# Kernel tuning notes

Measured on AMD Instinct MI355X. Metric: run time of the kernel, lower is better.

## Reference

```python
import jax, jax.numpy as jnp
import numpy as np
from jax import lax

B, C_IN, T_IN = 1024, 22, 2047
C_TEMP, KT, PAD = 20, 12, 6
N_PATCH = 8
ATT_OUT = 18
N_OUT = 4
BN_EPS = 1e-5
REEIG_EPS = 1e-4


def _sym(X):
    return 0.5 * (X + jnp.swapaxes(X, -1, -2))


def _eig_fn(X, fn):
    w, v = jnp.linalg.eigh(_sym(X))
    return jnp.einsum('...ij,...j,...kj->...ik', v, fn(w), v)


def _logm(X):
    return _eig_fn(X, lambda w: jnp.log(jnp.maximum(w, 1e-10)))


def _expm(X):
    return _eig_fn(X, jnp.exp)


def _reeig(X):
    return _eig_fn(X, lambda w: jnp.maximum(w, REEIG_EPS))


def _batchnorm(x, gamma, beta):
    # x: (B, C, T); training-mode stats over (B, T)
    mu = x.mean(axis=(0, 2), keepdims=True)
    var = x.var(axis=(0, 2), keepdims=True)
    return (x - mu) * jax.lax.rsqrt(var + BN_EPS) * gamma[None, :, None] + beta[None, :, None]


def setup_inputs() -> dict:
    key = jax.random.key(0)
    ks = jax.random.split(key, 8)
    tangent_dim = ATT_OUT * (ATT_OUT + 1) // 2
    return {
        'x': jax.random.normal(ks[0], (B, C_IN, T_IN), dtype=jnp.float32),
        'w_spat': jax.random.normal(ks[1], (C_IN, C_IN), dtype=jnp.float32) * 0.3,
        'b_spat': jnp.zeros((C_IN,), jnp.float32),
        'g1': jnp.ones((C_IN,), jnp.float32),
        'be1': jnp.zeros((C_IN,), jnp.float32),
        'w_temp': jax.random.normal(ks[2], (C_TEMP, C_IN, KT), dtype=jnp.float32) * 0.1,
        'b_temp': jnp.zeros((C_TEMP,), jnp.float32),
        'g2': jnp.ones((C_TEMP,), jnp.float32),
        'be2': jnp.zeros((C_TEMP,), jnp.float32),
        'wq': jax.random.normal(ks[3], (ATT_OUT, C_TEMP), dtype=jnp.float32) / np.sqrt(C_TEMP),
        'wk': jax.random.normal(ks[4], (ATT_OUT, C_TEMP), dtype=jnp.float32) / np.sqrt(C_TEMP),
        'wv': jax.random.normal(ks[5], (ATT_OUT, C_TEMP), dtype=jnp.float32) / np.sqrt(C_TEMP),
        'w_lin': jax.random.normal(ks[6], (N_OUT, N_PATCH * tangent_dim), dtype=jnp.float32) * 0.05,
        'b_lin': jnp.zeros((N_OUT,), jnp.float32),
    }


def _matt_forward(x, w_spat, b_spat, g1, be1, w_temp, b_temp, g2, be2, wq, wk, wv, w_lin, b_lin):
    b = x.shape[0]
    # spatial filter: Conv2d(1, n_chans, (n_chans,1)) == full channel mix
    h = jnp.einsum('oc,bct->bot', w_spat, x) + b_spat[None, :, None]
    h = _batchnorm(h, g1, be1)
    # temporal conv: Conv2d(n_chans, 20, (1,12), pad (0,6)) == 1D conv over time
    h = lax.conv_general_dilated(h, w_temp, window_strides=(1,), padding=[(PAD, PAD)],
                                 dimension_numbers=('NCH', 'OIH', 'NCH'))
    h = h + b_temp[None, :, None]
    h = _batchnorm(h, g2, be2)
    # patch embedding: split time into N_PATCH segments -> (B, P, C, Tp)
    cf, tt = h.shape[1], h.shape[2]
    tp = tt // N_PATCH
    h = h[:, :, :N_PATCH * tp].reshape(b, cf, N_PATCH, tp).transpose(0, 2, 1, 3)
    # sample covariance per patch + trace normalization
    hc = h - h.mean(axis=-1, keepdims=True)
    cov = jnp.einsum('bpct,bpdt->bpcd', hc, hc) / (tp - 1)
    cov = cov / jnp.trace(cov, axis1=-2, axis2=-1)[..., None, None]
    # manifold attention: BiMap Q/K/V = W X W^T
    Q = jnp.einsum('oi,bpij,qj->bpoq', wq, cov, wq)
    K = jnp.einsum('oi,bpij,qj->bpoq', wk, cov, wk)
    V = jnp.einsum('oi,bpij,qj->bpoq', wv, cov, wv)
    lq, lk, lv = _logm(Q), _logm(K), _logm(V)
    n = lq.shape[-1]
    fq = lq.reshape(b, N_PATCH, n * n)
    fk = lk.reshape(b, N_PATCH, n * n)
    sq = jnp.sum(fq * fq, -1)
    sk = jnp.sum(fk * fk, -1)
    cross = jnp.einsum('bid,bjd->bij', fq, fk)
    d2 = jnp.maximum(sq[:, :, None] + sk[:, None, :] - 2.0 * cross, 0.0)
    energy = jnp.sqrt(d2 + 1e-12)  # log-Euclidean distance ||logQ_i - logK_j||_F
    weights = 1.0 / (1.0 + jnp.log1p(energy))
    prob = jax.nn.softmax(weights, axis=-2)          # normalize over queries i
    probT = jnp.swapaxes(prob, -1, -2)               # (b, j, i)
    # log-Euclidean weighted Frechet mean: expm(sum_i w_ji logm(V_i))
    out = _expm(jnp.einsum('bji,bixy->bjxy', probT, lv))
    # R2E: ReEig + LogEig + triu vectorization (off-diag * sqrt(2))
    lt = _logm(_reeig(out))
    iu0, iu1 = np.triu_indices(n)
    scale = jnp.asarray(np.where(iu0 == iu1, 1.0, np.sqrt(2.0)), dtype=lt.dtype)
    vec = lt[..., iu0, iu1] * scale                  # (B, P, n(n+1)/2)
    feat = vec.reshape(b, -1)
    return feat @ w_lin.T + b_lin


def reference(x, w_spat, b_spat, g1, be1, w_temp, b_temp, g2, be2, wq, wk, wv, w_lin, b_lin):
    return _matt_forward(x, w_spat, b_spat, g1, be1, w_temp, b_temp, g2, be2, wq, wk, wv, w_lin, b_lin)
```

## Files before the change

### kernel.cpp

```cpp
#include <hip/hip_runtime.h>
#include <math.h>

constexpr int NSWEEP = 5;

constexpr size_t OFF_SUMX   = 0;
constexpr size_t OFF_G      = 22;
constexpr size_t OFF_SUM2   = 288;
constexpr size_t OFF_SUMSQ2 = 308;
constexpr size_t OFF_S2     = 328;
constexpr size_t OFF_A      = 352;
constexpr size_t OFF_D      = 840;
constexpr size_t OFF_WR     = 864;
constexpr size_t OFF_COV    = 6144;
constexpr size_t OFF_LQKV   = 3282944;
constexpr size_t OFF_FEAT   = 11245568;

struct Tri { int a[253]; int b[253]; };
constexpr Tri mk_tri(int n) {
    Tri t{}; int c = 0;
    for (int i = 0; i < n; ++i) for (int j = i; j < n; ++j) { t.a[c] = i; t.b[c] = j; ++c; }
    return t;
}
constexpr Tri T22 = mk_tri(22);
constexpr Tri T20 = mk_tri(20);
constexpr Tri T18 = mk_tri(18);

struct Sched { int p[17][9]; int q[17][9]; };
constexpr Sched mk_sched() {
    Sched s{};
    for (int r = 0; r < 17; ++r)
        for (int k = 0; k < 9; ++k) {
            int x, y;
            if (k == 0) { x = 17; y = r; }
            else { x = (r + k) % 17; y = (r - k + 17) % 17; }
            s.p[r][k] = x < y ? x : y;
            s.q[r][k] = x < y ? y : x;
        }
    return s;
}
constexpr Sched SCH = mk_sched();

__device__ __forceinline__ float jacobi18(float* __restrict__ a, float* __restrict__ v,
                                          int jj, int base) {
    int pt[17];
#pragma unroll
    for (int r = 0; r < 17; ++r) {
        int k1 = jj - r; if (k1 < 0) k1 += 17;
        int partner;
        if (jj == 17)      { partner = r; }
        else if (k1 == 0)  { partner = 17; }
        else if (k1 <= 8)  { partner = r - k1; if (partner < 0) partner += 17; }
        else               { partner = r + 17 - k1; if (partner >= 17) partner -= 17; }
        pt[r] = partner;
    }
    int kt[17];
#pragma unroll
    for (int r = 0; r < 17; ++r) {
        int k1 = jj - r; if (k1 < 0) k1 += 17;
        kt[r] = (jj == 17) ? 0 : (k1 == 0 ? 0 : (k1 <= 8 ? k1 : 17 - k1));
    }
    float mydiag = a[0];
#pragma unroll
    for (int i = 1; i < 18; ++i) if (jj == i) mydiag = a[i];

    for (int sw = 0; sw < NSWEEP; ++sw) {
#pragma unroll
        for (int r = 0; r < 17; ++r) {
            const int partner = pt[r];
            const int paddr = base + partner;
            const bool isp = jj < partner;
            float pd = __shfl(mydiag, paddr, 64);
            float apq = a[0];
#pragma unroll
            for (int i = 1; i < 18; ++i) if (partner == i) apq = a[i];
            float app = isp ? mydiag : pd;
            float aqq = isp ? pd : mydiag;
            float apqc = (fabsf(apq) < 1e-36f) ? 1e-36f : apq;
            float tau = (aqq - app) * 0.5f * __builtin_amdgcn_rcpf(apqc);
            float t0 = __builtin_amdgcn_rcpf(fabsf(tau) + __builtin_amdgcn_sqrtf(1.f + tau * tau));
            t0 = (tau < 0.f) ? -t0 : t0;
            float tb[9];
#pragma unroll
            for (int k = 0; k < 9; ++k)
                tb[k] = __shfl(t0, base + SCH.p[r][k], 64);
            float cc[9], ss[9];
#pragma unroll
            for (int k = 0; k < 9; ++k) {
                cc[k] = __builtin_amdgcn_rsqf(1.f + tb[k] * tb[k]);
                ss[k] = tb[k] * cc[k];
            }
            const int kk = kt[r];
            float mt = tb[0], mc = cc[0], ms = ss[0];
#pragma unroll
            for (int t2 = 1; t2 < 9; ++t2)
                if (kk == t2) { mt = tb[t2]; mc = cc[t2]; ms = ss[t2]; }
            mydiag = fmaf(isp ? -mt : mt, apq, mydiag);
#pragma unroll
            for (int k = 0; k < 9; ++k) {
                const int p = SCH.p[r][k], q = SCH.q[r][k];
                float tp = a[p], tq = a[q];
                a[p] = cc[k] * tp - ss[k] * tq;
                a[q] = ss[k] * tp + cc[k] * tq;
            }
            float ssig = isp ? -ms : ms;
#pragma unroll
            for (int i = 0; i < 18; ++i) {
                float oa = __shfl(a[i], paddr, 64);
                a[i] = mc * a[i] + ssig * oa;
            }
#pragma unroll
            for (int i = 0; i < 18; ++i) {
                float ov = __shfl(v[i], paddr, 64);
                v[i] = mc * v[i] + ssig * ov;
            }
        }
    }
    float lam = a[0];
#pragma unroll
    for (int i = 1; i < 18; ++i) if (jj == i) lam = a[i];
    return lam;
}

__global__ void k0_zero(float* ws) {
    int tid = threadIdx.x;
    for (int i = tid; i < 352; i += 256) ws[i] = 0.f;
}

__global__ __launch_bounds__(256) void k1_stats(const float* __restrict__ x,
                                                float* __restrict__ sumx,
                                                float* __restrict__ G) {
    int b = blockIdx.x, tid = threadIdx.x;
    __shared__ float xt[22 * 257];
    float accp = 0.f, accs = 0.f;
    int c1 = 0, c2 = 0;
    if (tid < 253) { c1 = T22.a[tid]; c2 = T22.b[tid]; }
    const float* xb = x + (size_t)b * 22 * 2047;
    for (int t0 = 0; t0 < 2047; t0 += 256) {
        __syncthreads();
        for (int idx = tid; idx < 22 * 256; idx += 256) {
            int c = idx >> 8, tl = idx & 255;
            int t = t0 + tl;
            xt[c * 257 + tl] = (t < 2047) ? xb[c * 2047 + t] : 0.f;
        }
        __syncthreads();
        if (tid < 253) {
            float s = 0.f;
            for (int t = 0; t < 256; ++t) s += xt[c1 * 257 + t] * xt[c2 * 257 + t];
            accp += s;
        }
        if (tid < 22) {
            float s = 0.f;
            for (int t = 0; t < 256; ++t) s += xt[tid * 257 + t];
            accs += s;
        }
    }
    if (tid < 253) atomicAdd(&G[tid], accp);
    if (tid < 22) atomicAdd(&sumx[tid], accs);
}

__global__ __launch_bounds__(256) void k2_prep(const float* __restrict__ w_spat,
                                               const float* __restrict__ b_spat,
                                               const float* __restrict__ g1,
                                               const float* __restrict__ be1,
                                               const float* __restrict__ w_temp,
                                               const float* __restrict__ sumx,
                                               const float* __restrict__ G,
                                               float* __restrict__ A,
                                               float* __restrict__ dv,
                                               float* __restrict__ w_r) {
    int tid = threadIdx.x;
    __shared__ float cov[22 * 22], mux[22], mu1s[22], s1s[22];
    const float invN = 1.f / (1024.f * 2047.f);
    if (tid < 22) mux[tid] = sumx[tid] * invN;
    __syncthreads();
    if (tid < 253) {
        int c1 = T22.a[tid], c2 = T22.b[tid];
        float cv = G[tid] * invN - mux[c1] * mux[c2];
        cov[c1 * 22 + c2] = cv; cov[c2 * 22 + c1] = cv;
    }
    __syncthreads();
    if (tid < 22) {
        int c = tid;
        float m = b_spat[c], varv = 0.f;
        for (int e = 0; e < 22; ++e) m += w_spat[c * 22 + e] * mux[e];
        for (int i = 0; i < 22; ++i) {
            float wi = w_spat[c * 22 + i];
            for (int j = 0; j < 22; ++j) varv += wi * w_spat[c * 22 + j] * cov[i * 22 + j];
        }
        mu1s[c] = m;
        s1s[c] = g1[c] * rsqrtf(varv + 1e-5f);
    }
    __syncthreads();
    for (int idx = tid; idx < 484; idx += 256) {
        int c = idx / 22;
        A[idx] = s1s[c] * w_spat[idx];
    }
    if (tid < 22) dv[tid] = s1s[tid] * (b_spat[tid] - mu1s[tid]) + be1[tid];
    for (int idx = tid; idx < 5280; idx += 256) {
        int f = idx / 264, r = idx % 264;
        w_r[r * 20 + f] = w_temp[idx];
    }
}

__global__ __launch_bounds__(256) void k3_conv(const float* __restrict__ x,
                                               const float* __restrict__ wsA,
                                               const float* __restrict__ wsd,
                                               const float* __restrict__ w_r,
                                               float* __restrict__ cov_raw,
                                               float* __restrict__ sum2,
                                               float* __restrict__ sumsq2) {
    int bp = blockIdx.x;
    int b = bp >> 3, p = bp & 7;
    int tid = threadIdx.x;
    __shared__ float xs[22 * 267];
    __shared__ float h2[20 * 257];
    __shared__ float pm[20];

    const float* xb = x + (size_t)b * 22 * 2047;
    const int t0 = p * 256 - 6;
    for (int idx = tid; idx < 22 * 267; idx += 256) {
        int c = idx / 267, tl = idx % 267;
        int t = t0 + tl;
        xs[idx] = (t >= 0 && t < 2047) ? xb[c * 2047 + t] : 0.f;
    }
    __syncthreads();
    for (int tl = tid; tl < 267; tl += 256) {
        float xv[22];
#pragma unroll
        for (int c = 0; c < 22; ++c) xv[c] = xs[c * 267 + tl];
        int t = t0 + tl;
        bool valid = (t >= 0 && t < 2047);
#pragma unroll
        for (int c = 0; c < 22; ++c) {
            float acc = wsd[c];
#pragma unroll
            for (int e = 0; e < 22; ++e) acc += wsA[c * 22 + e] * xv[e];
            xs[c * 267 + tl] = valid ? acc : 0.f;
        }
    }
    __syncthreads();
    {
        int tl = tid;
        float acc[20];
#pragma unroll
        for (int f = 0; f < 20; ++f) acc[f] = 0.f;
        for (int c = 0; c < 22; ++c) {
#pragma unroll
            for (int k = 0; k < 12; ++k) {
                float hv = xs[c * 267 + tl + k];
                const float* wp = w_r + (c * 12 + k) * 20;
#pragma unroll
                for (int f = 0; f < 20; ++f) acc[f] += wp[f] * hv;
            }
        }
#pragma unroll
        for (int f = 0; f < 20; ++f) h2[f * 257 + tl] = acc[f];
    }
    __syncthreads();
    if (tid < 20) {
        int f = tid;
        float s = 0.f, ss = 0.f;
        for (int t = 0; t < 256; ++t) { float v = h2[f * 257 + t]; s += v; ss += v * v; }
        pm[f] = s * (1.f / 256.f);
        atomicAdd(&sum2[f], s);
        atomicAdd(&sumsq2[f], ss);
    }
    __syncthreads();
    for (int pr = tid; pr < 210; pr += 256) {
        int f = T20.a[pr], g = T20.b[pr];
        float s = 0.f;
        for (int t = 0; t < 256; ++t) s += h2[f * 257 + t] * h2[g * 257 + t];
        float cv = s - 256.f * pm[f] * pm[g];
        cov_raw[(size_t)bp * 400 + f * 20 + g] = cv;
        if (f != g) cov_raw[(size_t)bp * 400 + g * 20 + f] = cv;
    }
}

__global__ void k4_s2(const float* __restrict__ g2, const float* __restrict__ sum2,
                      const float* __restrict__ sumsq2, float* __restrict__ s2) {
    int tid = threadIdx.x;
    if (tid < 20) {
        const float invN = 1.f / (1024.f * 2048.f);
        float mu = sum2[tid] * invN;
        float var = sumsq2[tid] * invN - mu * mu;
        s2[tid] = g2[tid] * rsqrtf(var + 1e-5f);
    }
}

__global__ __launch_bounds__(256) void k5_qkv(const float* __restrict__ wq,
                                              const float* __restrict__ wk,
                                              const float* __restrict__ wv,
                                              const float* __restrict__ s2g,
                                              const float* __restrict__ cov_raw,
                                              float* __restrict__ lqkv) {
    int tid = threadIdx.x;
    int wave = tid >> 6;
    int lane = tid & 63;
    int bp = blockIdx.x * 4 + wave;
    __shared__ float Wl[1080];
    __shared__ float s2l[20];
    __shared__ float covn[4][400];
    __shared__ float Vs[4][972];
    __shared__ float lws[4][54];

    if (tid < 20) s2l[tid] = s2g[tid];
    for (int idx = lane; idx < 400; idx += 64)
        covn[wave][idx] = cov_raw[(size_t)bp * 400 + idx];
    __syncthreads();
    for (int idx = tid; idx < 1080; idx += 256) {
        int m = idx / 360, rem = idx % 360;
        const float* W = (m == 0) ? wq : (m == 1) ? wk : wv;
        Wl[idx] = W[rem] * s2l[rem % 20];
    }
    __syncthreads();

    float tr = 0.f;
#pragma unroll
    for (int f = 0; f < 20; ++f) tr += covn[wave][f * 21] * s2l[f] * s2l[f];
    float trinv = 1.f / tr;

    int grp = lane / 18;
    int jj = lane - grp * 18;
    int m = grp < 3 ? grp : 2;
    int base = grp * 18;
    float Wrow[20];
#pragma unroll
    for (int d = 0; d < 20; ++d) Wrow[d] = Wl[m * 360 + jj * 20 + d];
    float u[20];
#pragma unroll
    for (int e = 0; e < 20; ++e) {
        float acc = 0.f;
#pragma unroll
        for (int d = 0; d < 20; ++d) acc += covn[wave][e * 20 + d] * Wrow[d];
        u[e] = acc;
    }
    float a[18], v[18];
#pragma unroll
    for (int i = 0; i < 18; ++i) {
        float acc = 0.f;
#pragma unroll
        for (int e = 0; e < 20; ++e) acc += Wl[m * 360 + i * 20 + e] * u[e];
        a[i] = acc * trinv;
        v[i] = (i == jj) ? 1.f : 0.f;
    }
    float lam = jacobi18(a, v, jj, base);
    float lw = __logf(fmaxf(lam, 1e-10f));
    if (grp < 3) {
#pragma unroll
        for (int i = 0; i < 18; ++i) Vs[wave][(m * 18 + i) * 18 + jj] = v[i];
        lws[wave][m * 18 + jj] = lw;
    }
    __builtin_amdgcn_wave_barrier();
    for (int idx = lane; idx < 972; idx += 64) {
        int m2 = idx / 324, rem = idx % 324, i = rem / 18, jo = rem % 18;
        float acc = 0.f;
#pragma unroll
        for (int kk = 0; kk < 18; ++kk)
            acc += Vs[wave][(m2 * 18 + i) * 18 + kk] * lws[wave][m2 * 18 + kk] * Vs[wave][(m2 * 18 + jo) * 18 + kk];
        lqkv[(size_t)(bp * 3 + m2) * 324 + rem] = acc;
    }
}

__global__ __launch_bounds__(256) void k6_attn(const float* __restrict__ lqkv,
                                               float* __restrict__ mixed) {
    int b = blockIdx.x, tid = threadIdx.x;
    __shared__ float L[7776];
    __shared__ float sq[8], sk[8], cross[64], prob[64];
    const float* src = lqkv + (size_t)b * 7776;
    for (int idx = tid; idx < 7776; idx += 256) L[idx] = src[idx];
    __syncthreads();
    if (tid < 64) {
        int i = tid >> 3, j = tid & 7;
        const float* fq = &L[(i * 3 + 0) * 324];
        const float* fk = &L[(j * 3 + 1) * 324];
        float cr = 0.f;
        for (int e = 0; e < 324; ++e) cr += fq[e] * fk[e];
        cross[tid] = cr;
    } else if (tid < 72) {
        int i = tid - 64;
        const float* fq = &L[(i * 3 + 0) * 324];
        float s = 0.f;
        for (int e = 0; e < 324; ++e) s += fq[e] * fq[e];
        sq[i] = s;
    } else if (tid < 80) {
        int i = tid - 72;
        const float* fk = &L[(i * 3 + 1) * 324];
        float s = 0.f;
        for (int e = 0; e < 324; ++e) s += fk[e] * fk[e];
        sk[i] = s;
    }
    __syncthreads();
    if (tid < 8) {
        int j = tid;
        float w[8], mx = -1e30f;
        for (int i = 0; i < 8; ++i) {
            float d2 = fmaxf(sq[i] + sk[j] - 2.f * cross[i * 8 + j], 0.0f);
            float en = sqrtf(d2 + 1e-12f);
            w[i] = 1.f / (1.f + log1pf(en));
            mx = fmaxf(mx, w[i]);
        }
        float ssum = 0.f;
        for (int i = 0; i < 8; ++i) { w[i] = __expf(w[i] - mx); ssum += w[i]; }
        float inv = 1.f / ssum;
        for (int i = 0; i < 8; ++i) prob[i * 8 + j] = w[i] * inv;
    }
    __syncthreads();
    float* dst = mixed + (size_t)b * 8 * 324;
    for (int idx = tid; idx < 8 * 324; idx += 256) {
        int j = idx / 324, e = idx % 324;
        float acc = 0.f;
#pragma unroll
        for (int i = 0; i < 8; ++i) acc += prob[i * 8 + j] * L[(i * 3 + 2) * 324 + e];
        dst[idx] = acc;
    }
}

__global__ __launch_bounds__(256) void k7_post(const float* __restrict__ mixed,
                                               float* __restrict__ feat) {
    int tid = threadIdx.x;
    int wave = tid >> 6;
    int lane = tid & 63;
    int blk = blockIdx.x;
    int grp = lane / 18;
    int jj = lane - grp * 18;
    int m = grp < 3 ? grp : 2;
    int base = grp * 18;
    int mat = blk * 12 + wave * 3 + m;
    int matc = mat < 8192 ? mat : 8191;
    __shared__ float Vs[4][972];
    __shared__ float lws[4][54];

    const float* src = mixed + (size_t)matc * 324;
    float a[18], v[18];
#pragma unroll
    for (int i = 0; i < 18; ++i) {
        a[i] = src[i * 18 + jj];
        v[i] = (i == jj) ? 1.f : 0.f;
    }
    float diag = a[0], asum = 0.f;
#pragma unroll
    for (int i = 0; i < 18; ++i) {
        if (jj == i) diag = a[i];
        asum += fabsf(a[i]);
    }
    float gb = 2.f * diag - asum;
#pragma unroll
    for (int off = 32; off; off >>= 1) gb = fminf(gb, __shfl_xor(gb, off, 64));
    const bool skipAll = (gb > -9.2103f);

    if (!skipAll) {
        float lam = jacobi18(a, v, jj, base);
        float lw = fmaxf(lam, -9.210340371976182f);
        if (grp < 3) {
#pragma unroll
            for (int i = 0; i < 18; ++i) Vs[wave][(m * 18 + i) * 18 + jj] = v[i];
            lws[wave][m * 18 + jj] = lw;
        }
    }
    __builtin_amdgcn_wave_barrier();
    for (int idx = lane; idx < 513; idx += 64) {
        int m2 = idx / 171, rem = idx % 171;
        int mat2 = blk * 12 + wave * 3 + m2;
        if (mat2 >= 8192) continue;
        int i = T18.a[rem], jo = T18.b[rem];
        float acc;
        if (skipAll) {
            acc = mixed[(size_t)mat2 * 324 + i * 18 + jo];
        } else {
            acc = 0.f;
#pragma unroll
            for (int kk = 0; kk < 18; ++kk)
                acc += Vs[wave][(m2 * 18 + i) * 18 + kk] * lws[wave][m2 * 18 + kk] * Vs[wave][(m2 * 18 + jo) * 18 + kk];
        }
        float scl = (i == jo) ? 1.f : 1.41421356237309515f;
        int bb = mat2 >> 3, pp = mat2 & 7;
        feat[(size_t)bb * 1368 + pp * 171 + rem] = acc * scl;
    }
}

__global__ __launch_bounds__(256) void k8_lin(const float* __restrict__ feat,
                                              const float* __restrict__ w_lin,
                                              const float* __restrict__ b_lin,
                                              float* __restrict__ out) {
    int b = blockIdx.x, tid = threadIdx.x;
    int o = tid >> 6, lane = tid & 63;
    const float* fb = feat + (size_t)b * 1368;
    const float* wo = w_lin + o * 1368;
    float acc = 0.f;
    for (int e = lane; e < 1368; e += 64) acc += fb[e] * wo[e];
    for (int off = 32; off; off >>= 1) acc += __shfl_down(acc, off, 64);
    if (lane == 0) out[b * 4 + o] = acc + b_lin[o];
}

extern "C" void kernel_launch(void* const* d_in, const int* in_sizes, int n_in,
                              void* d_out, int out_size, void* d_ws, size_t ws_size,
                              hipStream_t stream) {
    (void)in_sizes; (void)n_in; (void)out_size; (void)ws_size;
    const float* x      = (const float*)d_in[0];
    const float* w_spat = (const float*)d_in[1];
    const float* b_spat = (const float*)d_in[2];
    const float* g1     = (const float*)d_in[3];
    const float* be1    = (const float*)d_in[4];
    const float* w_temp = (const float*)d_in[5];
    const float* g2     = (const float*)d_in[7];
    const float* wq     = (const float*)d_in[9];
    const float* wk     = (const float*)d_in[10];
    const float* wv     = (const float*)d_in[11];
    const float* w_lin  = (const float*)d_in[12];
    const float* b_lin  = (const float*)d_in[13];
    float* ws  = (float*)d_ws;
    float* out = (float*)d_out;

    k0_zero<<<1, 256, 0, stream>>>(ws);
    k1_stats<<<1024, 256, 0, stream>>>(x, ws + OFF_SUMX, ws + OFF_G);
    k2_prep<<<1, 256, 0, stream>>>(w_spat, b_spat, g1, be1, w_temp,
                                   ws + OFF_SUMX, ws + OFF_G,
                                   ws + OFF_A, ws + OFF_D, ws + OFF_WR);
    k3_conv<<<8192, 256, 0, stream>>>(x, ws + OFF_A, ws + OFF_D, ws + OFF_WR,
                                      ws + OFF_COV, ws + OFF_SUM2, ws + OFF_SUMSQ2);
    k4_s2<<<1, 64, 0, stream>>>(g2, ws + OFF_SUM2, ws + OFF_SUMSQ2, ws + OFF_S2);
    k5_qkv<<<2048, 256, 0, stream>>>(wq, wk, wv, ws + OFF_S2, ws + OFF_COV, ws + OFF_LQKV);
    k6_attn<<<1024, 256, 0, stream>>>(ws + OFF_LQKV, ws + OFF_COV );
    k7_post<<<683, 256, 0, stream>>>(ws + OFF_COV, ws + OFF_FEAT);
    k8_lin<<<1024, 256, 0, stream>>>(ws + OFF_FEAT, w_lin, b_lin, out);
}
```

Baseline: 1.654 ms.

## Store eigenvectors as rows and stage Jacobi matrix columns in LDS

The Jacobi eigen-solver now keeps each lane's eigenvector row and applies the column rotations locally, removing the 18 cross-lane shuffles per rotation step that the old eigenvector update needed. Diagonal and off-diagonal entries are read from a per-wave LDS copy of the matrix that is rewritten after each step, replacing register select chains. Cos/sin values are computed inline and the partner table is packed into bytes to reduce register pressure. The change adds LDS stores of the full column every step and relies on wave-level barriers for correctness. Shared buffers in k5 and k7 are merged into a padded per-wave arena.

```diff
diff --git a/kernel.cpp b/kernel.cpp
--- a/kernel.cpp
+++ b/kernel.cpp
@@ -40,9 +40,10 @@
 }
 constexpr Sched SCH = mk_sched();
 
-__device__ __forceinline__ float jacobi18(float* __restrict__ a, float* __restrict__ v,
-                                          int jj, int base) {
-    int pt[17];
+__device__ __forceinline__ float jacobi18(float* __restrict__ a, float* __restrict__ vr,
+                                          int jj, int base, float* __restrict__ scr,
+                                          int sgbase) {
+    unsigned ptP[5] = {0u, 0u, 0u, 0u, 0u};
 #pragma unroll
     for (int r = 0; r < 17; ++r) {
         int k1 = jj - r; if (k1 < 0) k1 += 17;
@@ -51,56 +52,52 @@
         else if (k1 == 0)  { partner = 17; }
         else if (k1 <= 8)  { partner = r - k1; if (partner < 0) partner += 17; }
         else               { partner = r + 17 - k1; if (partner >= 17) partner -= 17; }
-        pt[r] = partner;
-    }
-    int kt[17];
-#pragma unroll
-    for (int r = 0; r < 17; ++r) {
-        int k1 = jj - r; if (k1 < 0) k1 += 17;
-        kt[r] = (jj == 17) ? 0 : (k1 == 0 ? 0 : (k1 <= 8 ? k1 : 17 - k1));
-    }
-    float mydiag = a[0];
-#pragma unroll
-    for (int i = 1; i < 18; ++i) if (jj == i) mydiag = a[i];
-
+        ptP[r >> 2] |= (unsigned)partner << ((r & 3) * 8);
+    }
+    const int mycol = (sgbase + jj) * 20;
+    const bool wrt = base < 54;
+    if (wrt) {
+        float4* d4 = (float4*)(scr + mycol);
+        d4[0] = make_float4(a[0],  a[1],  a[2],  a[3]);
+        d4[1] = make_float4(a[4],  a[5],  a[6],  a[7]);
+        d4[2] = make_float4(a[8],  a[9],  a[10], a[11]);
+        d4[3] = make_float4(a[12], a[13], a[14], a[15]);
+        *(float2*)(scr + mycol + 16) = make_float2(a[16], a[17]);
+    }
     for (int sw = 0; sw < NSWEEP; ++sw) {
 #pragma unroll
         for (int r = 0; r < 17; ++r) {
-            const int partner = pt[r];
+            const int partner = (int)((ptP[r >> 2] >> ((r & 3) * 8)) & 0xffu);
             const int paddr = base + partner;
             const bool isp = jj < partner;
-            float pd = __shfl(mydiag, paddr, 64);
-            float apq = a[0];
-#pragma unroll
-            for (int i = 1; i < 18; ++i) if (partner == i) apq = a[i];
-            float app = isp ? mydiag : pd;
-            float aqq = isp ? pd : mydiag;
+            const int plane = isp ? jj : partner;
+            float apq  = scr[mycol + partner];
+            float mydg = scr[mycol + jj];
+            float pdg  = scr[(sgbase + partner) * 20 + partner];
+            float app = isp ? mydg : pdg;
+            float aqq = isp ? pdg : mydg;
             float apqc = (fabsf(apq) < 1e-36f) ? 1e-36f : apq;
             float tau = (aqq - app) * 0.5f * __builtin_amdgcn_rcpf(apqc);
-            float t0 = __builtin_amdgcn_rcpf(fabsf(tau) + __builtin_amdgcn_sqrtf(1.f + tau * tau));
+            float t0 = __builtin_amdgcn_rcpf(fabsf(tau) + __builtin_amdgcn_sqrtf(fmaf(tau, tau, 1.f)));
             t0 = (tau < 0.f) ? -t0 : t0;
             float tb[9];
 #pragma unroll
             for (int k = 0; k < 9; ++k)
                 tb[k] = __shfl(t0, base + SCH.p[r][k], 64);
-            float cc[9], ss[9];
-#pragma unroll
-            for (int k = 0; k < 9; ++k) {
-                cc[k] = __builtin_amdgcn_rsqf(1.f + tb[k] * tb[k]);
-                ss[k] = tb[k] * cc[k];
-            }
-            const int kk = kt[r];
-            float mt = tb[0], mc = cc[0], ms = ss[0];
-#pragma unroll
-            for (int t2 = 1; t2 < 9; ++t2)
-                if (kk == t2) { mt = tb[t2]; mc = cc[t2]; ms = ss[t2]; }
-            mydiag = fmaf(isp ? -mt : mt, apq, mydiag);
+            float mt = __shfl(t0, base + plane, 64);
+            float mc = __builtin_amdgcn_rsqf(fmaf(mt, mt, 1.f));
+            float ms = mt * mc;
 #pragma unroll
             for (int k = 0; k < 9; ++k) {
                 const int p = SCH.p[r][k], q = SCH.q[r][k];
+                float c = __builtin_amdgcn_rsqf(fmaf(tb[k], tb[k], 1.f));
+                float s = tb[k] * c;
                 float tp = a[p], tq = a[q];
-                a[p] = cc[k] * tp - ss[k] * tq;
-                a[q] = ss[k] * tp + cc[k] * tq;
+                a[p] = c * tp - s * tq;
+                a[q] = s * tp + c * tq;
+                float vp = vr[p], vq = vr[q];
+                vr[p] = c * vp - s * vq;
+                vr[q] = s * vp + c * vq;
             }
             float ssig = isp ? -ms : ms;
 #pragma unroll
@@ -108,17 +105,17 @@
                 float oa = __shfl(a[i], paddr, 64);
                 a[i] = mc * a[i] + ssig * oa;
             }
-#pragma unroll
-            for (int i = 0; i < 18; ++i) {
-                float ov = __shfl(v[i], paddr, 64);
-                v[i] = mc * v[i] + ssig * ov;
+            if (wrt) {
+                float4* d4 = (float4*)(scr + mycol);
+                d4[0] = make_float4(a[0],  a[1],  a[2],  a[3]);
+                d4[1] = make_float4(a[4],  a[5],  a[6],  a[7]);
+                d4[2] = make_float4(a[8],  a[9],  a[10], a[11]);
+                d4[3] = make_float4(a[12], a[13], a[14], a[15]);
+                *(float2*)(scr + mycol + 16) = make_float2(a[16], a[17]);
             }
         }
     }
-    float lam = a[0];
-#pragma unroll
-    for (int i = 1; i < 18; ++i) if (jj == i) lam = a[i];
-    return lam;
+    return scr[mycol + jj];
 }
 
 __global__ void k0_zero(float* ws) {
@@ -299,13 +296,12 @@
     int bp = blockIdx.x * 4 + wave;
     __shared__ float Wl[1080];
     __shared__ float s2l[20];
-    __shared__ float covn[4][400];
-    __shared__ float Vs[4][972];
-    __shared__ float lws[4][54];
+    __shared__ __align__(16) float arena[4][1136];
+    float* wsh = arena[wave];
 
     if (tid < 20) s2l[tid] = s2g[tid];
     for (int idx = lane; idx < 400; idx += 64)
-        covn[wave][idx] = cov_raw[(size_t)bp * 400 + idx];
+        wsh[idx] = cov_raw[(size_t)bp * 400 + idx];
     __syncthreads();
     for (int idx = tid; idx < 1080; idx += 256) {
         int m = idx / 360, rem = idx % 360;
@@ -316,7 +312,7 @@
 
     float tr = 0.f;
 #pragma unroll
-    for (int f = 0; f < 20; ++f) tr += covn[wave][f * 21] * s2l[f] * s2l[f];
+    for (int f = 0; f < 20; ++f) tr += wsh[f * 21] * s2l[f] * s2l[f];
     float trinv = 1.f / tr;
 
     int grp = lane / 18;
@@ -331,24 +327,30 @@
     for (int e = 0; e < 20; ++e) {
         float acc = 0.f;
 #pragma unroll
-        for (int d = 0; d < 20; ++d) acc += covn[wave][e * 20 + d] * Wrow[d];
+        for (int d = 0; d < 20; ++d) acc += wsh[e * 20 + d] * Wrow[d];
         u[e] = acc;
     }
-    float a[18], v[18];
+    float a[18], vr[18];
 #pragma unroll
     for (int i = 0; i < 18; ++i) {
         float acc = 0.f;
 #pragma unroll
         for (int e = 0; e < 20; ++e) acc += Wl[m * 360 + i * 20 + e] * u[e];
         a[i] = acc * trinv;
-        v[i] = (i == jj) ? 1.f : 0.f;
-    }
-    float lam = jacobi18(a, v, jj, base);
+        vr[i] = (i == jj) ? 1.f : 0.f;
+    }
+    __builtin_amdgcn_wave_barrier();
+    float lam = jacobi18(a, vr, jj, base, wsh, m * 18);
     float lw = __logf(fmaxf(lam, 1e-10f));
+    __builtin_amdgcn_wave_barrier();
     if (grp < 3) {
-#pragma unroll
-        for (int i = 0; i < 18; ++i) Vs[wave][(m * 18 + i) * 18 + jj] = v[i];
-        lws[wave][m * 18 + jj] = lw;
+        float* vd = wsh + (m * 18 + jj) * 20;
+        ((float4*)vd)[0] = make_float4(vr[0],  vr[1],  vr[2],  vr[3]);
+        ((float4*)vd)[1] = make_float4(vr[4],  vr[5],  vr[6],  vr[7]);
+        ((float4*)vd)[2] = make_float4(vr[8],  vr[9],  vr[10], vr[11]);
+        ((float4*)vd)[3] = make_float4(vr[12], vr[13], vr[14], vr[15]);
+        *(float2*)(vd + 16) = make_float2(vr[16], vr[17]);
+        wsh[1080 + m * 18 + jj] = lw;
     }
     __builtin_amdgcn_wave_barrier();
     for (int idx = lane; idx < 972; idx += 64) {
@@ -356,7 +358,7 @@
         float acc = 0.f;
 #pragma unroll
         for (int kk = 0; kk < 18; ++kk)
-            acc += Vs[wave][(m2 * 18 + i) * 18 + kk] * lws[wave][m2 * 18 + kk] * Vs[wave][(m2 * 18 + jo) * 18 + kk];
+            acc += wsh[(m2 * 18 + i) * 20 + kk] * wsh[1080 + m2 * 18 + kk] * wsh[(m2 * 18 + jo) * 20 + kk];
         lqkv[(size_t)(bp * 3 + m2) * 324 + rem] = acc;
     }
 }
@@ -427,15 +429,15 @@
     int base = grp * 18;
     int mat = blk * 12 + wave * 3 + m;
     int matc = mat < 8192 ? mat : 8191;
-    __shared__ float Vs[4][972];
-    __shared__ float lws[4][54];
+    __shared__ __align__(16) float arena[4][1136];
+    float* wsh = arena[wave];
 
     const float* src = mixed + (size_t)matc * 324;
-    float a[18], v[18];
+    float a[18], vr[18];
 #pragma unroll
     for (int i = 0; i < 18; ++i) {
         a[i] = src[i * 18 + jj];
-        v[i] = (i == jj) ? 1.f : 0.f;
+        vr[i] = (i == jj) ? 1.f : 0.f;
     }
     float diag = a[0], asum = 0.f;
 #pragma unroll
@@ -449,12 +451,16 @@
     const bool skipAll = (gb > -9.2103f);
 
     if (!skipAll) {
-        float lam = jacobi18(a, v, jj, base);
+        float lam = jacobi18(a, vr, jj, base, wsh, m * 18);
         float lw = fmaxf(lam, -9.210340371976182f);
         if (grp < 3) {
-#pragma unroll
-            for (int i = 0; i < 18; ++i) Vs[wave][(m * 18 + i) * 18 + jj] = v[i];
-            lws[wave][m * 18 + jj] = lw;
+            float* vd = wsh + (m * 18 + jj) * 20;
+            ((float4*)vd)[0] = make_float4(vr[0],  vr[1],  vr[2],  vr[3]);
+            ((float4*)vd)[1] = make_float4(vr[4],  vr[5],  vr[6],  vr[7]);
+            ((float4*)vd)[2] = make_float4(vr[8],  vr[9],  vr[10], vr[11]);
+            ((float4*)vd)[3] = make_float4(vr[12], vr[13], vr[14], vr[15]);
+            *(float2*)(vd + 16) = make_float2(vr[16], vr[17]);
+            wsh[1080 + m * 18 + jj] = lw;
         }
     }
     __builtin_amdgcn_wave_barrier();
@@ -470,7 +476,7 @@
             acc = 0.f;
 #pragma unroll
             for (int kk = 0; kk < 18; ++kk)
-                acc += Vs[wave][(m2 * 18 + i) * 18 + kk] * lws[wave][m2 * 18 + kk] * Vs[wave][(m2 * 18 + jo) * 18 + kk];
+                acc += wsh[(m2 * 18 + i) * 20 + kk] * wsh[1080 + m2 * 18 + kk] * wsh[(m2 * 18 + jo) * 20 + kk];
         }
         float scl = (i == jo) ? 1.f : 1.41421356237309515f;
         int bb = mat2 >> 3, pp = mat2 & 7;
```

Result: slower. 2.024 ms (+22.4%).

## Store Jacobi eigenvectors row-wise per lane to drop cross-lane shuffles

Applied to the files above, without the earlier changes.

The eigenvector matrix is now held transposed, one row per lane, so each Jacobi rotation updates it with local register arithmetic using the broadcast rotation coefficients. This removes 18 cross-lane shuffles per rotation step. The per-lane rotation parameter is now fetched with one shuffle and a recomputed rsqrt instead of a selection table, and the shared-memory store of eigenvectors is transposed to match. It adds 36 FMAs per rotation in exchange for the removed shuffles.

```diff
diff --git a/kernel.cpp b/kernel.cpp
--- a/kernel.cpp
+++ b/kernel.cpp
@@ -40,7 +40,7 @@
 }
 constexpr Sched SCH = mk_sched();
 
-__device__ __forceinline__ float jacobi18(float* __restrict__ a, float* __restrict__ v,
+__device__ __forceinline__ float jacobi18(float* __restrict__ a, float* __restrict__ vr,
                                           int jj, int base) {
     int pt[17];
 #pragma unroll
@@ -53,12 +53,6 @@
         else               { partner = r + 17 - k1; if (partner >= 17) partner -= 17; }
         pt[r] = partner;
     }
-    int kt[17];
-#pragma unroll
-    for (int r = 0; r < 17; ++r) {
-        int k1 = jj - r; if (k1 < 0) k1 += 17;
-        kt[r] = (jj == 17) ? 0 : (k1 == 0 ? 0 : (k1 <= 8 ? k1 : 17 - k1));
-    }
     float mydiag = a[0];
 #pragma unroll
     for (int i = 1; i < 18; ++i) if (jj == i) mydiag = a[i];
@@ -69,6 +63,7 @@
             const int partner = pt[r];
             const int paddr = base + partner;
             const bool isp = jj < partner;
+            const int plane = isp ? jj : partner;
             float pd = __shfl(mydiag, paddr, 64);
             float apq = a[0];
 #pragma unroll
@@ -77,7 +72,7 @@
             float aqq = isp ? pd : mydiag;
             float apqc = (fabsf(apq) < 1e-36f) ? 1e-36f : apq;
             float tau = (aqq - app) * 0.5f * __builtin_amdgcn_rcpf(apqc);
-            float t0 = __builtin_amdgcn_rcpf(fabsf(tau) + __builtin_amdgcn_sqrtf(1.f + tau * tau));
+            float t0 = __builtin_amdgcn_rcpf(fabsf(tau) + __builtin_amdgcn_sqrtf(fmaf(tau, tau, 1.f)));
             t0 = (tau < 0.f) ? -t0 : t0;
             float tb[9];
 #pragma unroll
@@ -86,14 +81,12 @@
             float cc[9], ss[9];
 #pragma unroll
             for (int k = 0; k < 9; ++k) {
-                cc[k] = __builtin_amdgcn_rsqf(1.f + tb[k] * tb[k]);
+                cc[k] = __builtin_amdgcn_rsqf(fmaf(tb[k], tb[k], 1.f));
                 ss[k] = tb[k] * cc[k];
             }
-            const int kk = kt[r];
-            float mt = tb[0], mc = cc[0], ms = ss[0];
-#pragma unroll
-            for (int t2 = 1; t2 < 9; ++t2)
-                if (kk == t2) { mt = tb[t2]; mc = cc[t2]; ms = ss[t2]; }
+            float mt = __shfl(t0, base + plane, 64);
+            float mc = __builtin_amdgcn_rsqf(fmaf(mt, mt, 1.f));
+            float ms = mt * mc;
             mydiag = fmaf(isp ? -mt : mt, apq, mydiag);
 #pragma unroll
             for (int k = 0; k < 9; ++k) {
@@ -101,17 +94,15 @@
                 float tp = a[p], tq = a[q];
                 a[p] = cc[k] * tp - ss[k] * tq;
                 a[q] = ss[k] * tp + cc[k] * tq;
+                float vp = vr[p], vq = vr[q];
+                vr[p] = cc[k] * vp - ss[k] * vq;
+                vr[q] = ss[k] * vp + cc[k] * vq;
             }
             float ssig = isp ? -ms : ms;
 #pragma unroll
             for (int i = 0; i < 18; ++i) {
                 float oa = __shfl(a[i], paddr, 64);
                 a[i] = mc * a[i] + ssig * oa;
-            }
-#pragma unroll
-            for (int i = 0; i < 18; ++i) {
-                float ov = __shfl(v[i], paddr, 64);
-                v[i] = mc * v[i] + ssig * ov;
             }
         }
     }
@@ -334,20 +325,20 @@
         for (int d = 0; d < 20; ++d) acc += covn[wave][e * 20 + d] * Wrow[d];
         u[e] = acc;
     }
-    float a[18], v[18];
+    float a[18], vr[18];
 #pragma unroll
     for (int i = 0; i < 18; ++i) {
         float acc = 0.f;
 #pragma unroll
         for (int e = 0; e < 20; ++e) acc += Wl[m * 360 + i * 20 + e] * u[e];
         a[i] = acc * trinv;
-        v[i] = (i == jj) ? 1.f : 0.f;
-    }
-    float lam = jacobi18(a, v, jj, base);
+        vr[i] = (i == jj) ? 1.f : 0.f;
+    }
+    float lam = jacobi18(a, vr, jj, base);
     float lw = __logf(fmaxf(lam, 1e-10f));
     if (grp < 3) {
 #pragma unroll
-        for (int i = 0; i < 18; ++i) Vs[wave][(m * 18 + i) * 18 + jj] = v[i];
+        for (int i = 0; i < 18; ++i) Vs[wave][(m * 18 + jj) * 18 + i] = vr[i];
         lws[wave][m * 18 + jj] = lw;
     }
     __builtin_amdgcn_wave_barrier();
@@ -431,11 +422,11 @@
     __shared__ float lws[4][54];
 
     const float* src = mixed + (size_t)matc * 324;
-    float a[18], v[18];
+    float a[18], vr[18];
 #pragma unroll
     for (int i = 0; i < 18; ++i) {
         a[i] = src[i * 18 + jj];
-        v[i] = (i == jj) ? 1.f : 0.f;
+        vr[i] = (i == jj) ? 1.f : 0.f;
     }
     float diag = a[0], asum = 0.f;
 #pragma unroll
@@ -449,11 +440,11 @@
     const bool skipAll = (gb > -9.2103f);
 
     if (!skipAll) {
-        float lam = jacobi18(a, v, jj, base);
+        float lam = jacobi18(a, vr, jj, base);
         float lw = fmaxf(lam, -9.210340371976182f);
         if (grp < 3) {
 #pragma unroll
-            for (int i = 0; i < 18; ++i) Vs[wave][(m * 18 + i) * 18 + jj] = v[i];
+            for (int i = 0; i < 18; ++i) Vs[wave][(m * 18 + jj) * 18 + i] = vr[i];
             lws[wave][m * 18 + jj] = lw;
         }
     }
```

After: 1.960 ms. 18.5% more time.
